# Kernel optimization log

Measured on AMD Instinct MI355X. Metric: run time of the kernel, lower is better.

Reference implementation:

```python
import jax, jax.numpy as jnp
import numpy as np

L = 4          # num_layers
DIM = 256      # model dim
HEADS = 8
DH = DIM // HEADS
WINDOW = 512   # sliding window size
FF = 4 * DIM
EPS = 1e-5


def setup_inputs() -> dict:
    key = jax.random.key(0)
    ks = jax.random.split(key, 13)
    B, S = 1, 4096
    s = 0.02
    inp = {
        "x": jax.random.normal(ks[0], (B, S, DIM), jnp.float32),
        # per-layer stacked weights (leading axis = layer) for lax.scan
        "wq": jax.random.normal(ks[1], (L, DIM, DIM), jnp.float32) * s,
        "bq": jnp.zeros((L, DIM), jnp.float32),
        "wk": jax.random.normal(ks[2], (L, DIM, DIM), jnp.float32) * s,
        "bk": jnp.zeros((L, DIM), jnp.float32),
        "wv": jax.random.normal(ks[3], (L, DIM, DIM), jnp.float32) * s,
        "bv": jnp.zeros((L, DIM), jnp.float32),
        "wo": jax.random.normal(ks[4], (L, DIM, DIM), jnp.float32) * s,
        "bo": jnp.zeros((L, DIM), jnp.float32),
        "w1": jax.random.normal(ks[5], (L, DIM, FF), jnp.float32) * s,
        "b1": jnp.zeros((L, FF), jnp.float32),
        "w2": jax.random.normal(ks[6], (L, FF, DIM), jnp.float32) * s,
        "b2": jnp.zeros((L, DIM), jnp.float32),
    }
    return inp


def _ln(x):
    # LayerNorm with elementwise_affine=False
    m = jnp.mean(x, axis=-1, keepdims=True)
    v = jnp.var(x, axis=-1, keepdims=True)
    return (x - m) / jnp.sqrt(v + EPS)


def reference(x, wq, bq, wk, bk, wv, bv, wo, bo, w1, b1, w2, b2):
    B, S, D = x.shape
    idx = jnp.arange(S)
    # sliding window mask: |q_idx - kv_idx| <= window_size // 2
    mask = jnp.abs(idx[:, None] - idx[None, :]) <= (WINDOW // 2)  # [S, S]
    neg = jnp.finfo(x.dtype).min
    scale = 1.0 / np.sqrt(DH)

    def layer(h, p):
        lwq, lbq, lwk, lbk, lwv, lbv, lwo, lbo, lw1, lb1, lw2, lb2 = p
        # pre-norm self-attention residual
        n = _ln(h)
        q = (n @ lwq + lbq).reshape(B, S, HEADS, DH)
        k = (n @ lwk + lbk).reshape(B, S, HEADS, DH)
        v = (n @ lwv + lbv).reshape(B, S, HEADS, DH)
        scores = jnp.einsum('bqhd,bkhd->bhqk', q, k) * scale
        scores = jnp.where(mask, scores, neg)
        attn = jax.nn.softmax(scores, axis=-1)
        o = jnp.einsum('bhqk,bkhd->bqhd', attn, v).reshape(B, S, D)
        h = h + o @ lwo + lbo
        # post-norm dense residual: x = norm(x); x = x + ffn(x)
        h = _ln(h)
        h = h + jax.nn.gelu(h @ lw1 + lb1) @ lw2 + lb2
        return h, None

    x, _ = jax.lax.scan(layer, x, (wq, bq, wk, bk, wv, bv, wo, bo, w1, b1, w2, b2))
    return x
```

## Files before the change

kernel.cpp:

```cpp
#include <hip/hip_runtime.h>
#include <math.h>

#define SEQ 4096
#define DIM 256
#define NH 8
#define DHD 32
#define FFD 1024
#define NLAYER 4

typedef unsigned short ushort_t;
typedef __attribute__((ext_vector_type(8))) short bf16x8;
typedef __attribute__((ext_vector_type(4))) float f32x4;

__device__ __forceinline__ float gelu_f(float x){
  const float c = 0.7978845608028654f;
  float x3 = x*x*x;
  return 0.5f * x * (1.0f + tanhf(c*(x + 0.044715f*x3)));
}

__device__ __forceinline__ ushort_t f2b(float f){
  union { float f; unsigned u; } x; x.f = f;
  unsigned r = x.u + 0x7FFF + ((x.u >> 16) & 1);
  return (ushort_t)(r >> 16);
}

__device__ __forceinline__ void gload16(void* lds, const void* g){
  __builtin_amdgcn_global_load_lds((const __attribute__((address_space(1))) void*)g,
                                   (__attribute__((address_space(3))) void*)lds, 16, 0, 0);
}

__global__ __launch_bounds__(256) void wconv_kernel(
    const float* __restrict__ wq, const float* __restrict__ wk,
    const float* __restrict__ wv, const float* __restrict__ wo,
    const float* __restrict__ w1, const float* __restrict__ w2,
    ushort_t* __restrict__ wt){
  __shared__ ushort_t tile[64][65];
  int b = blockIdx.x, tid = threadIdx.x;
  const float* src; ushort_t* dst; int K, N, tk, tn;
  if (b < 256){
    int m = b>>6, rem = b&63, l = rem>>4, t = rem&15;
    K = 256; N = 256; tk = t>>2; tn = t&3;
    const float* s4 = (m==0)?wq:(m==1)?wk:(m==2)?wv:wo;
    src = s4 + (size_t)l*65536;
    dst = wt + (size_t)(m*NLAYER + l)*65536;
  } else if (b < 512){
    int rem = b-256, l = rem>>6, t = rem&63;
    K = 256; N = 1024; tk = t>>4; tn = t&15;
    src = w1 + (size_t)l*262144;
    dst = wt + 1048576 + (size_t)l*262144;
  } else {
    int rem = b-512, l = rem>>6, t = rem&63;
    K = 1024; N = 256; tk = t>>2; tn = t&3;
    src = w2 + (size_t)l*262144;
    dst = wt + 2097152 + (size_t)l*262144;
  }
  int k0 = tk*64, n0 = tn*64;
  #pragma unroll
  for (int i=0;i<16;i++){
    int idx = tid + 256*i, row = idx>>6, col = idx&63;
    tile[row][col] = f2b(src[(size_t)(k0+row)*N + n0+col]);
  }
  __syncthreads();
  #pragma unroll
  for (int i=0;i<16;i++){
    int idx = tid + 256*i, nrow = idx>>6, kcol = idx&63;
    dst[(size_t)(n0+nrow)*K + k0+kcol] = tile[kcol][nrow];
  }
}

__global__ __launch_bounds__(256) void ln_kernel(const float* __restrict__ x,
    float* __restrict__ yf, ushort_t* __restrict__ yb){
  int row  = blockIdx.x*4 + (threadIdx.x>>6);
  int lane = threadIdx.x & 63;
  const float4* xr = (const float4*)(x + (size_t)row*DIM);
  float4 v = xr[lane];
  float s  = v.x+v.y+v.z+v.w;
  float sq = v.x*v.x+v.y*v.y+v.z*v.z+v.w*v.w;
  #pragma unroll
  for(int off=32; off>0; off>>=1){
    s  += __shfl_down(s, off);
    sq += __shfl_down(sq, off);
  }
  s = __shfl(s, 0); sq = __shfl(sq, 0);
  float mean = s * (1.0f/DIM);
  float var  = sq * (1.0f/DIM) - mean*mean;
  float rinv = rsqrtf(var + 1e-5f);
  float4 o;
  o.x=(v.x-mean)*rinv; o.y=(v.y-mean)*rinv; o.z=(v.z-mean)*rinv; o.w=(v.w-mean)*rinv;
  if (yf) ((float4*)(yf + (size_t)row*DIM))[lane] = o;
  if (yb){
    ushort_t* yp = yb + (size_t)row*DIM + lane*4;
    yp[0]=f2b(o.x); yp[1]=f2b(o.y); yp[2]=f2b(o.z); yp[3]=f2b(o.w);
  }
}

__global__ __launch_bounds__(256) void gemm_kernel(
    const ushort_t* __restrict__ A, const ushort_t* __restrict__ Wt,
    const float* __restrict__ bias, const float* __restrict__ R,
    float* __restrict__ Cf, ushort_t* __restrict__ Cb,
    int M, int N, int K, int act){
  __shared__ ushort_t As[32*256];
  __shared__ ushort_t Bs[64*256];
  int tid = threadIdx.x;
  int w = tid>>6, lane = tid&63;
  int wr = w>>1, wc = w&1;
  int q4 = lane>>4, u = lane&15;
  int m0 = blockIdx.y*32, n0 = blockIdx.x*64;
  f32x4 acc[2];
  acc[0] = (f32x4){0.f,0.f,0.f,0.f};
  acc[1] = (f32x4){0.f,0.f,0.f,0.f};

  for (int k0 = 0; k0 < K; k0 += 256){
    if (k0) __syncthreads();
    #pragma unroll
    for (int i=0;i<4;i++){
      int idx = tid + 256*i;
      int row = idx>>5, ch = idx&31;
      gload16(&As[idx*8], &A[(size_t)(m0+row)*K + k0 + ((ch^(row&7))*8)]);
    }
    #pragma unroll
    for (int i=0;i<8;i++){
      int idx = tid + 256*i;
      int row = idx>>5, ch = idx&31;
      gload16(&Bs[idx*8], &Wt[(size_t)(n0+row)*K + k0 + ((ch^(row&7))*8)]);
    }
    __syncthreads();
    #pragma unroll
    for (int kk=0;kk<8;kk++){
      int ar = wr*16 + u;
      bf16x8 af = *(const bf16x8*)&As[ar*256 + (((kk*4+q4)^(ar&7))*8)];
      #pragma unroll
      for (int j=0;j<2;j++){
        int br = wc*32 + j*16 + u;
        bf16x8 bf = *(const bf16x8*)&Bs[br*256 + (((kk*4+q4)^(br&7))*8)];
        acc[j] = __builtin_amdgcn_mfma_f32_16x16x32_bf16(af, bf, acc[j], 0, 0, 0);
      }
    }
  }
  #pragma unroll
  for (int j=0;j<2;j++){
    #pragma unroll
    for (int t=0;t<4;t++){
      int m = m0 + wr*16 + q4*4 + t;
      int n = n0 + wc*32 + j*16 + u;
      float val = acc[j][t] + bias[n];
      if (R)   val += R[(size_t)m*N + n];
      if (act) val = gelu_f(val);
      if (Cf)  Cf[(size_t)m*N + n] = val;
      if (Cb)  Cb[(size_t)m*N + n] = f2b(val);
    }
  }
}

__global__ __launch_bounds__(256) void qkv_kernel(
    const float* __restrict__ hin,
    const ushort_t* __restrict__ wtq, const ushort_t* __restrict__ wtk, const ushort_t* __restrict__ wtv,
    const float* __restrict__ bqp, const float* __restrict__ bkp, const float* __restrict__ bvp,
    ushort_t* __restrict__ qo, ushort_t* __restrict__ ko, ushort_t* __restrict__ vo){
  __shared__ ushort_t As[32*256];
  __shared__ ushort_t Bs[64*256];
  int tid = threadIdx.x;
  int w = tid>>6, lane = tid&63;
  int wr = w>>1, wc = w&1;
  int q4 = lane>>4, u = lane&15;
  int m0 = blockIdx.y*32, n0 = blockIdx.x*64;

  #pragma unroll
  for (int i=0;i<8;i++){
    int idx = tid + 256*i;
    int row = idx>>5, ch = idx&31;
    gload16(&Bs[idx*8], &wtq[(size_t)(n0+row)*DIM + ((ch^(row&7))*8)]);
  }
  #pragma unroll
  for (int r=0;r<8;r++){
    int row = w*8 + r;
    float4 v = *(const float4*)&hin[(size_t)(m0+row)*DIM + lane*4];
    float s  = v.x+v.y+v.z+v.w;
    float sq = v.x*v.x+v.y*v.y+v.z*v.z+v.w*v.w;
    #pragma unroll
    for (int off=32; off>0; off>>=1){ s += __shfl_down(s,off); sq += __shfl_down(sq,off); }
    s = __shfl(s,0); sq = __shfl(sq,0);
    float mean = s*(1.0f/DIM), var = sq*(1.0f/DIM) - mean*mean;
    float rinv = rsqrtf(var + 1e-5f);
    int ch = lane>>1, half = lane&1;
    ushort4 o4;
    o4.x = f2b((v.x-mean)*rinv); o4.y = f2b((v.y-mean)*rinv);
    o4.z = f2b((v.z-mean)*rinv); o4.w = f2b((v.w-mean)*rinv);
    *(ushort4*)&As[row*256 + ((ch^(row&7))*8 + half*4)] = o4;
  }
  __syncthreads();

  #pragma unroll
  for (int z=0; z<3; z++){
    const float* bias = (z==0)?bqp:(z==1)?bkp:bvp;
    ushort_t* Cb      = (z==0)?qo :(z==1)?ko :vo;
    f32x4 acc[2];
    acc[0]=(f32x4){0.f,0.f,0.f,0.f}; acc[1]=(f32x4){0.f,0.f,0.f,0.f};
    #pragma unroll
    for (int kk=0;kk<8;kk++){
      int ar = wr*16 + u;
      bf16x8 af = *(const bf16x8*)&As[ar*256 + (((kk*4+q4)^(ar&7))*8)];
      #pragma unroll
      for (int j=0;j<2;j++){
        int br = wc*32 + j*16 + u;
        bf16x8 bf = *(const bf16x8*)&Bs[br*256 + (((kk*4+q4)^(br&7))*8)];
        acc[j] = __builtin_amdgcn_mfma_f32_16x16x32_bf16(af, bf, acc[j], 0, 0, 0);
      }
    }
    if (z < 2){
      __syncthreads();
      const ushort_t* Wn = (z==0)?wtk:wtv;
      #pragma unroll
      for (int i=0;i<8;i++){
        int idx = tid + 256*i;
        int row = idx>>5, ch = idx&31;
        gload16(&Bs[idx*8], &Wn[(size_t)(n0+row)*DIM + ((ch^(row&7))*8)]);
      }
    }
    #pragma unroll
    for (int j=0;j<2;j++)
      #pragma unroll
      for (int t=0;t<4;t++){
        int m = m0 + wr*16 + q4*4 + t;
        int n = n0 + wc*32 + j*16 + u;
        Cb[(size_t)m*DIM + n] = f2b(acc[j][t] + bias[n]);
      }
    if (z < 2) __syncthreads();
  }
}

__global__ __launch_bounds__(256) void attn_kernel(
    const ushort_t* __restrict__ q, const ushort_t* __restrict__ k,
    const ushort_t* __restrict__ v, ushort_t* __restrict__ out){
  int q0 = blockIdx.x * 64;
  int h  = blockIdx.y;
  int tid = threadIdx.x;
  int w = tid >> 6;
  int lane = tid & 63;
  int u = lane & 15, q4 = lane >> 4;

  __shared__ ushort_t Ks[2][64][40];
  __shared__ ushort_t Vt[2][32][72];
  __shared__ ushort_t Pw[4][16][72];

  bf16x8 aq = *(const bf16x8*)(q + (size_t)(q0 + w*16 + u)*DIM + h*DHD + q4*8);

  float m[4], l[4];
  f32x4 acc[2];
  #pragma unroll
  for (int t=0;t<4;t++){ m[t] = -INFINITY; l[t] = 0.f; }
  acc[0] = (f32x4){0.f,0.f,0.f,0.f};
  acc[1] = (f32x4){0.f,0.f,0.f,0.f};

  const float sl2 = 0.25510703448358519f;

  int lo = q0 - 256; if (lo < 0) lo = 0;
  int hi = q0 + 63 + 256; if (hi > SEQ-1) hi = SEQ-1;
  int kt0 = (lo >> 6) << 6;
  int kt1 = (hi >> 6) << 6;

  int key = tid >> 2, d0 = (tid & 3) * 8;
  int vd0 = w * 8;

  bf16x8 kr = *(const bf16x8*)(k + (size_t)(kt0+key)*DIM + h*DHD + d0);
  bf16x8 vr = *(const bf16x8*)(v + (size_t)(kt0+lane)*DIM + h*DHD + vd0);
  *(bf16x8*)&Ks[0][key][d0] = kr;
  #pragma unroll
  for (int j=0;j<8;j++) Vt[0][vd0+j][lane] = (ushort_t)vr[j];

  int p = 0;
  for (int kt = kt0; kt <= kt1; kt += 64, p ^= 1){
    __syncthreads();
    bool have_next = (kt + 64 <= kt1);
    if (have_next){
      kr = *(const bf16x8*)(k + (size_t)(kt+64+key)*DIM + h*DHD + d0);
      vr = *(const bf16x8*)(v + (size_t)(kt+64+lane)*DIM + h*DHD + vd0);
    }

    f32x4 sc[4];
    #pragma unroll
    for (int t4=0;t4<4;t4++){
      bf16x8 bk = *(const bf16x8*)&Ks[p][t4*16 + u][q4*8];
      sc[t4] = __builtin_amdgcn_mfma_f32_16x16x32_bf16(aq, bk, (f32x4){0.f,0.f,0.f,0.f}, 0, 0, 0);
    }

    bool needs_mask = (kt < q0-192) || (kt > q0+192);
    #pragma unroll
    for (int t=0;t<4;t++){
      float mx = -INFINITY;
      if (needs_mask){
        int q_idx = q0 + w*16 + q4*4 + t;
        #pragma unroll
        for (int t4=0;t4<4;t4++){
          float s = sc[t4][t] * sl2;
          int k_idx = kt + t4*16 + u;
          int diff = q_idx - k_idx; if (diff < 0) diff = -diff;
          if (diff > 256) s = -INFINITY;
          sc[t4][t] = s;
          mx = fmaxf(mx, s);
        }
      } else {
        #pragma unroll
        for (int t4=0;t4<4;t4++){
          float s = sc[t4][t] * sl2;
          sc[t4][t] = s;
          mx = fmaxf(mx, s);
        }
      }
      mx = fmaxf(mx, __shfl_xor(mx, 1));
      mx = fmaxf(mx, __shfl_xor(mx, 2));
      mx = fmaxf(mx, __shfl_xor(mx, 4));
      mx = fmaxf(mx, __shfl_xor(mx, 8));
      float nm = fmaxf(m[t], mx);
      float al = exp2f(m[t] - nm);
      float rs = 0.f;
      #pragma unroll
      for (int t4=0;t4<4;t4++){
        float pv = exp2f(sc[t4][t] - nm);
        rs += pv;
        Pw[w][q4*4+t][t4*16+u] = f2b(pv);
      }
      rs += __shfl_xor(rs, 1);
      rs += __shfl_xor(rs, 2);
      rs += __shfl_xor(rs, 4);
      rs += __shfl_xor(rs, 8);
      l[t] = l[t]*al + rs;
      m[t] = nm;
      acc[0][t] *= al;
      acc[1][t] *= al;
    }
    #pragma unroll
    for (int kk=0;kk<2;kk++){
      bf16x8 ap = *(const bf16x8*)&Pw[w][u][kk*32 + q4*8];
      #pragma unroll
      for (int d=0; d<2; d++){
        bf16x8 bvf = *(const bf16x8*)&Vt[p][d*16 + u][kk*32 + q4*8];
        acc[d] = __builtin_amdgcn_mfma_f32_16x16x32_bf16(ap, bvf, acc[d], 0, 0, 0);
      }
    }
    if (have_next){
      *(bf16x8*)&Ks[p^1][key][d0] = kr;
      #pragma unroll
      for (int j=0;j<8;j++) Vt[p^1][vd0+j][lane] = (ushort_t)vr[j];
    }
  }

  float rl[4];
  #pragma unroll
  for (int t=0;t<4;t++) rl[t] = 1.0f / l[t];
  #pragma unroll
  for (int d=0; d<2; d++)
    #pragma unroll
    for (int t=0;t<4;t++)
      out[(size_t)(q0 + w*16 + q4*4 + t)*DIM + h*DHD + d*16 + u] = f2b(acc[d][t]*rl[t]);
}

extern "C" void kernel_launch(void* const* d_in, const int* in_sizes, int n_in,
                              void* d_out, int out_size, void* d_ws, size_t ws_size,
                              hipStream_t stream) {
  const float* x  = (const float*)d_in[0];
  const float* wq = (const float*)d_in[1];
  const float* bq = (const float*)d_in[2];
  const float* wk = (const float*)d_in[3];
  const float* bk = (const float*)d_in[4];
  const float* wv = (const float*)d_in[5];
  const float* bv = (const float*)d_in[6];
  const float* wo = (const float*)d_in[7];
  const float* bo = (const float*)d_in[8];
  const float* w1 = (const float*)d_in[9];
  const float* b1 = (const float*)d_in[10];
  const float* w2 = (const float*)d_in[11];
  const float* b2 = (const float*)d_in[12];
  float* out = (float*)d_out;
  float* ws  = (float*)d_ws;

  ushort_t* wt    = (ushort_t*)ws;
  ushort_t* abuf  = (ushort_t*)(ws + 1572864);
  ushort_t* ffbf  = (ushort_t*)(ws + 2097152);
  float* qb = ws + 4194304;
  float* kb = ws + 5242880;
  float* vb = ws + 6291456;
  float* hb = ws + 7340032;
  ushort_t* qbh = (ushort_t*)qb;
  ushort_t* kbh = (ushort_t*)kb;
  ushort_t* vbh = (ushort_t*)vb;

  const ushort_t* w1t_base = wt + 1048576;
  const ushort_t* w2t_base = wt + 2097152;

  const dim3 blk(256);
  wconv_kernel<<<768, blk, 0, stream>>>(wq, wk, wv, wo, w1, w2, wt);

  for (int l = 0; l < NLAYER; l++){
    const float* hin = (l == 0) ? x : hb;
    const ushort_t* lwq = wt + (size_t)(0*NLAYER + l)*65536;
    const ushort_t* lwk = wt + (size_t)(1*NLAYER + l)*65536;
    const ushort_t* lwv = wt + (size_t)(2*NLAYER + l)*65536;
    const ushort_t* lwo = wt + (size_t)(3*NLAYER + l)*65536;
    const ushort_t* lw1 = w1t_base + (size_t)l*262144;
    const ushort_t* lw2 = w2t_base + (size_t)l*262144;

    qkv_kernel<<<dim3(4,128), blk, 0, stream>>>(hin, lwq, lwk, lwv,
        bq + (size_t)l*DIM, bk + (size_t)l*DIM, bv + (size_t)l*DIM, qbh, kbh, vbh);
    attn_kernel<<<dim3(SEQ/64, NH), blk, 0, stream>>>(qbh, kbh, vbh, abuf);
    gemm_kernel<<<dim3(4,128), blk, 0, stream>>>(abuf, lwo, bo + (size_t)l*DIM,
        hin, qb, nullptr, SEQ, DIM, DIM, 0);
    ln_kernel<<<SEQ/4, blk, 0, stream>>>(qb, kb, abuf);
    gemm_kernel<<<dim3(16,128), blk, 0, stream>>>(abuf, lw1, b1 + (size_t)l*FFD,
        nullptr, nullptr, ffbf, SEQ, FFD, DIM, 1);
    float* hout = (l == NLAYER-1) ? out : hb;
    gemm_kernel<<<dim3(4,128), blk, 0, stream>>>(ffbf, lw2, b2 + (size_t)l*DIM,
        kb, hout, nullptr, SEQ, DIM, FFD, 0);
  }
}
```

Before: 360.5 us.

## Add XCD-aware block swizzle and weight-stationary FFN1 kernel

Introduces an XCD swizzle that remaps flat block ids so that consecutive logical tiles land on the same chiplet, applied to gemm, qkv and attention kernels to improve L2 locality. It also replaces the FFN1 gemm launch with a dedicated kernel that loads one 64-column weight tile into LDS once and loops over four 32-row activation tiles. This is meant to cut redundant weight loads and the number of blocks. The trade-off is fewer blocks (512 instead of 2048) and serialized loads inside each block with no overlap. The swizzle hardcodes nwg=512, which matches every grid it is applied to.

Measured after the change: 343.6 us, median of 2. 1.05x faster.

```diff
diff --git a/kernel.cpp b/kernel.cpp
--- a/kernel.cpp
+++ b/kernel.cpp
@@ -27,6 +27,10 @@
 __device__ __forceinline__ void gload16(void* lds, const void* g){
   __builtin_amdgcn_global_load_lds((const __attribute__((address_space(1))) void*)g,
                                    (__attribute__((address_space(3))) void*)lds, 16, 0, 0);
+}
+
+__device__ __forceinline__ int xcd_swz(int b, int nwg){
+  return (b & 7)*(nwg >> 3) + (b >> 3);
 }
 
 __global__ __launch_bounds__(256) void wconv_kernel(
@@ -105,7 +109,8 @@
   int w = tid>>6, lane = tid&63;
   int wr = w>>1, wc = w&1;
   int q4 = lane>>4, u = lane&15;
-  int m0 = blockIdx.y*32, n0 = blockIdx.x*64;
+  int fid = xcd_swz(blockIdx.y*4 + blockIdx.x, 512);
+  int m0 = (fid>>2)*32, n0 = (fid&3)*64;
   f32x4 acc[2];
   acc[0] = (f32x4){0.f,0.f,0.f,0.f};
   acc[1] = (f32x4){0.f,0.f,0.f,0.f};
@@ -149,6 +154,58 @@
       if (Cf)  Cf[(size_t)m*N + n] = val;
       if (Cb)  Cb[(size_t)m*N + n] = f2b(val);
     }
+  }
+}
+
+__global__ __launch_bounds__(256) void ffn1m_kernel(
+    const ushort_t* __restrict__ A, const ushort_t* __restrict__ Wt,
+    const float* __restrict__ bias, ushort_t* __restrict__ Cb){
+  __shared__ ushort_t As[32*256];
+  __shared__ ushort_t Bs[64*256];
+  int tid = threadIdx.x;
+  int w = tid>>6, lane = tid&63;
+  int wr = w>>1, wc = w&1;
+  int q4 = lane>>4, u = lane&15;
+  int fid = xcd_swz(blockIdx.y*16 + blockIdx.x, 512);
+  int n0 = (fid & 15)*64;
+  int mg = (fid >> 4);
+  #pragma unroll
+  for (int i=0;i<8;i++){
+    int idx = tid + 256*i;
+    int row = idx>>5, ch = idx&31;
+    gload16(&Bs[idx*8], &Wt[(size_t)(n0+row)*DIM + ((ch^(row&7))*8)]);
+  }
+  for (int ms=0; ms<4; ms++){
+    int m0 = mg*128 + ms*32;
+    #pragma unroll
+    for (int i=0;i<4;i++){
+      int idx = tid + 256*i;
+      int row = idx>>5, ch = idx&31;
+      gload16(&As[idx*8], &A[(size_t)(m0+row)*DIM + ((ch^(row&7))*8)]);
+    }
+    __syncthreads();
+    f32x4 acc[2];
+    acc[0]=(f32x4){0.f,0.f,0.f,0.f}; acc[1]=(f32x4){0.f,0.f,0.f,0.f};
+    #pragma unroll
+    for (int kk=0;kk<8;kk++){
+      int ar = wr*16 + u;
+      bf16x8 af = *(const bf16x8*)&As[ar*256 + (((kk*4+q4)^(ar&7))*8)];
+      #pragma unroll
+      for (int j=0;j<2;j++){
+        int br = wc*32 + j*16 + u;
+        bf16x8 bf = *(const bf16x8*)&Bs[br*256 + (((kk*4+q4)^(br&7))*8)];
+        acc[j] = __builtin_amdgcn_mfma_f32_16x16x32_bf16(af, bf, acc[j], 0, 0, 0);
+      }
+    }
+    #pragma unroll
+    for (int j=0;j<2;j++)
+      #pragma unroll
+      for (int t=0;t<4;t++){
+        int m = m0 + wr*16 + q4*4 + t;
+        int n = n0 + wc*32 + j*16 + u;
+        Cb[(size_t)m*FFD + n] = f2b(gelu_f(acc[j][t] + bias[n]));
+      }
+    if (ms < 3) __syncthreads();
   }
 }
 
@@ -163,7 +220,8 @@
   int w = tid>>6, lane = tid&63;
   int wr = w>>1, wc = w&1;
   int q4 = lane>>4, u = lane&15;
-  int m0 = blockIdx.y*32, n0 = blockIdx.x*64;
+  int fid = xcd_swz(blockIdx.y*4 + blockIdx.x, 512);
+  int m0 = (fid>>2)*32, n0 = (fid&3)*64;
 
   #pragma unroll
   for (int i=0;i<8;i++){
@@ -232,8 +290,9 @@
 __global__ __launch_bounds__(256) void attn_kernel(
     const ushort_t* __restrict__ q, const ushort_t* __restrict__ k,
     const ushort_t* __restrict__ v, ushort_t* __restrict__ out){
-  int q0 = blockIdx.x * 64;
-  int h  = blockIdx.y;
+  int fid = xcd_swz(blockIdx.y*64 + blockIdx.x, 512);
+  int q0 = (fid & 63) * 64;
+  int h  = fid >> 6;
   int tid = threadIdx.x;
   int w = tid >> 6;
   int lane = tid & 63;
@@ -406,8 +465,8 @@
     gemm_kernel<<<dim3(4,128), blk, 0, stream>>>(abuf, lwo, bo + (size_t)l*DIM,
         hin, qb, nullptr, SEQ, DIM, DIM, 0);
     ln_kernel<<<SEQ/4, blk, 0, stream>>>(qb, kb, abuf);
-    gemm_kernel<<<dim3(16,128), blk, 0, stream>>>(abuf, lw1, b1 + (size_t)l*FFD,
-        nullptr, nullptr, ffbf, SEQ, FFD, DIM, 1);
+    ffn1m_kernel<<<dim3(16,32), blk, 0, stream>>>(abuf, lw1, b1 + (size_t)l*FFD,
+        ffbf);
     float* hout = (l == NLAYER-1) ? out : hb;
     gemm_kernel<<<dim3(4,128), blk, 0, stream>>>(ffbf, lw2, b2 + (size_t)l*DIM,
         kb, hout, nullptr, SEQ, DIM, FFD, 0);
```
